# Performance work log

Measured on AMD Instinct MI355X. Metric: run time of the kernel, lower is better.

Reference implementation:

```python
import jax, jax.numpy as jnp
import numpy as np

# Dimensions inferred from the module (few-shot reweighted YOLOv2 region loss)
B, C, NA, NCPA = 64, 20, 5, 1          # batch, base classes, anchors, classes-per-anchor
H, W = 19, 19                           # feature map (608 input / stride 32)
T = 50                                  # cfg.max_boxes
THRESH = 0.6
COORD_SCALE = 1.0
CLASS_SCALE = 1.0
NB = B * C                              # per-class 'image' rows, as in the torch code
A4 = NA * H * W
EPS = 1e-12
BCE_EPS = 1e-7
ANCHORS = [[1.3221, 1.73145], [3.19275, 4.00944], [5.05587, 8.09892], [9.47112, 4.84053], [11.2364, 10.0071]]


def iou_xywh(x1, y1, w1, h1, x2, y2, w2, h2):
    # center-size IoU, matches darknet bbox_iou(x1y1x2y2=False)
    l = jnp.maximum(x1 - w1 * 0.5, x2 - w2 * 0.5)
    r = jnp.minimum(x1 + w1 * 0.5, x2 + w2 * 0.5)
    t = jnp.maximum(y1 - h1 * 0.5, y2 - h2 * 0.5)
    b = jnp.minimum(y1 + h1 * 0.5, y2 + h2 * 0.5)
    inter = jnp.clip(r - l, 0.0) * jnp.clip(b - t, 0.0)
    union = w1 * h1 + w2 * h2 - inter
    return inter / jnp.maximum(union, EPS)


def setup_inputs() -> dict:
    key = jax.random.key(0)
    k1, k2, k3, k4 = jax.random.split(key, 4)
    output = jax.random.normal(k1, (NB, NA * (5 + NCPA), H, W), jnp.float32) * 0.5
    # target rows: [cls, x, y, w, h] * T, coords in (0,1); x kept > 0 so all boxes are 'valid'
    cls_ids = jax.random.randint(k2, (B, C, T), 0, C).astype(jnp.float32)
    xy = jax.random.uniform(k3, (B, C, T, 2), minval=0.05, maxval=0.95)
    wh = jax.random.uniform(k4, (B, C, T, 2), minval=0.05, maxval=0.5)
    target = jnp.concatenate([cls_ids[..., None], xy, wh], axis=-1).reshape(B, C, T * 5)
    anchors = jnp.asarray(ANCHORS, jnp.float32)
    return {"output": output, "target": target, "anchors": anchors}


def _forward(output, target, anchors):
    target = jax.lax.stop_gradient(target)
    anchors = jax.lax.stop_gradient(anchors)
    out5 = output.reshape(NB, NA, 5 + NCPA, H, W)
    x = jax.nn.sigmoid(out5[:, :, 0])
    y = jax.nn.sigmoid(out5[:, :, 1])
    w = out5[:, :, 2]
    h = out5[:, :, 3]
    conf = jax.nn.sigmoid(out5[:, :, 4])
    # class logits regrouped to original batch: (B*NA*H*W, C)
    cls = out5[:, :, 5:5 + NCPA].reshape(NB, NA, H, W)
    cls_logits = cls.reshape(B, C, NA * H * W).transpose(0, 2, 1).reshape(-1, C)
    # decode pred boxes (detached, mirroring torch's use of .data)
    grid_x = jnp.arange(W, dtype=jnp.float32)[None, None, None, :]
    grid_y = jnp.arange(H, dtype=jnp.float32)[None, None, :, None]
    aw = anchors[:, 0][None, :, None, None]
    ah = anchors[:, 1][None, :, None, None]
    px = jax.lax.stop_gradient(x) + grid_x
    py = jax.lax.stop_gradient(y) + grid_y
    pw = jnp.exp(jax.lax.stop_gradient(w)) * aw
    ph = jnp.exp(jax.lax.stop_gradient(h)) * ah
    # ground-truth boxes per row
    tgt = target.reshape(NB, T, 5)
    cls_t = tgt[:, :, 0]
    gx = tgt[:, :, 1] * W
    gy = tgt[:, :, 2] * H
    gw = tgt[:, :, 3] * W
    gh = tgt[:, :, 4] * H
    # 'break on first zero x' semantics
    valid = jnp.cumprod((tgt[:, :, 1] != 0).astype(jnp.int32), axis=1) > 0
    # stage 1: zero conf_mask where any gt IoU > thresh (scan over T to avoid (NB,T,A4) blowup)
    pxf = px.reshape(NB, A4); pyf = py.reshape(NB, A4)
    pwf = pw.reshape(NB, A4); phf = ph.reshape(NB, A4)

    def iou_step(ci, xs):
        gxt, gyt, gwt, ght, vt = xs
        iou = iou_xywh(pxf, pyf, pwf, phf, gxt[:, None], gyt[:, None], gwt[:, None], ght[:, None])
        return jnp.maximum(ci, jnp.where(vt[:, None], iou, 0.0)), None

    cur_ious, _ = jax.lax.scan(iou_step, jnp.zeros((NB, A4), jnp.float32), (gx.T, gy.T, gw.T, gh.T, valid.T))
    conf_mask0 = jnp.where(cur_ious.reshape(NB, NA, H, W) > THRESH, 0.0, 1.0)
    # best anchor per gt by wh-only IoU
    inter = jnp.minimum(gw[..., None], anchors[:, 0]) * jnp.minimum(gh[..., None], anchors[:, 1])
    union = gw[..., None] * gh[..., None] + anchors[:, 0] * anchors[:, 1] - inter
    best_n = jnp.argmax(inter / jnp.maximum(union, EPS), axis=-1).astype(jnp.int32)  # (NB,T)
    gi = gx.astype(jnp.int32)
    gj = gy.astype(jnp.int32)
    # stage 2: ordered scatter of targets (later boxes overwrite earlier, as in the torch loops)
    binds = jnp.arange(NB)
    z = jnp.zeros((NB, NA, H, W), jnp.float32)
    # seen < 12800 branch: tx=ty=0.5, tw=th=0, coord_mask=1
    carry0 = (jnp.ones_like(z), z, conf_mask0, jnp.full_like(z, 0.5), jnp.full_like(z, 0.5), z, z, z, z)

    def tgt_step(carry, xs):
        cm, clm, cfm, tx, ty, tw, th, tconf, tcls = carry
        gxt, gyt, gwt, ght, bn, git, gjt, vt, ct = xs
        idx = (binds, bn, gjt, git)

        def upd(arr, val):
            return arr.at[idx].set(jnp.where(vt, val, arr[idx]))

        aw_b = anchors[bn, 0]
        ah_b = anchors[bn, 1]
        iou = iou_xywh(gxt, gyt, gwt, ght, px[idx], py[idx], pw[idx], ph[idx])
        cm = upd(cm, 1.0)
        clm = upd(clm, 1.0)
        cfm = upd(cfm, 1.0)
        tx = upd(tx, gxt - git.astype(jnp.float32))
        ty = upd(ty, gyt - gjt.astype(jnp.float32))
        tw = upd(tw, jnp.log(jnp.maximum(gwt, EPS) / aw_b))
        th = upd(th, jnp.log(jnp.maximum(ght, EPS) / ah_b))
        tconf = upd(tconf, iou)
        tcls = upd(tcls, ct)
        return (cm, clm, cfm, tx, ty, tw, th, tconf, tcls), None

    xs = (gx.T, gy.T, gw.T, gh.T, best_n.T, gi.T, gj.T, valid.T, cls_t.T)
    (coord_mask, cls_mask, conf_mask, tx, ty, tw, th, tconf, tcls), _ = jax.lax.scan(tgt_step, carry0, xs)
    # regroup per-class rows back to original batch (neg_ratio='full' -> counts[i] == C)
    cm_grp = cls_mask.reshape(B, C, NA, H, W).sum(axis=1)
    tcls_grp = tcls.reshape(B, C, NA, H, W).sum(axis=1)
    sel = (cm_grp == 1.0).reshape(-1)           # exclude colliding cells
    labels = tcls_grp.reshape(-1).astype(jnp.int32)

    def bce_mean(p, t):
        p = jnp.clip(p, BCE_EPS, 1.0 - BCE_EPS)
        return jnp.mean(-(t * jnp.log(p) + (1.0 - t) * jnp.log(1.0 - p)))

    loss_x = COORD_SCALE * bce_mean(x * coord_mask, tx * coord_mask)
    loss_y = COORD_SCALE * bce_mean(y * coord_mask, ty * coord_mask)
    loss_w = COORD_SCALE * 0.5 * jnp.mean((w * coord_mask - tw * coord_mask) ** 2)
    loss_h = COORD_SCALE * 0.5 * jnp.mean((h * coord_mask - th * coord_mask) ** 2)
    loss_conf = 0.5 * jnp.mean((conf * conf_mask - tconf * conf_mask) ** 2)
    logp = jax.nn.log_softmax(cls_logits, axis=-1)
    nll = -jnp.take_along_axis(logp, labels[:, None], axis=1)[:, 0]
    nsel = jnp.maximum(jnp.sum(sel.astype(jnp.float32)), 1.0)
    loss_cls = CLASS_SCALE * jnp.sum(jnp.where(sel, nll, 0.0)) / nsel
    return loss_x + loss_y + loss_w + loss_h + loss_conf + loss_cls


def reference(output, target, anchors):
    return _forward(output, target, anchors)
```

## Files before the change

kernel.cpp:

```cpp
#include <hip/hip_runtime.h>
#include <math.h>

constexpr int cB   = 64;
constexpr int cC   = 20;
constexpr int cNA  = 5;
constexpr int cH   = 19;
constexpr int cW   = 19;
constexpr int cT   = 50;
constexpr int cNB  = cB * cC;
constexpr int cHW  = cH * cW;
constexpr int cA4  = cNA * cHW;
constexpr int cCH  = cNA * 6;
constexpr long cNTOT = (long)cNB * cA4;
constexpr int cCLS_BLOCKS = cB * cNA;

__device__ __constant__ float cAW[cNA]   = {1.3221f, 3.19275f, 5.05587f, 9.47112f, 11.2364f};
__device__ __constant__ float cAH[cNA]   = {1.73145f, 4.00944f, 8.09892f, 4.84053f, 10.0071f};
__device__ __constant__ float cAREA[cNA] = {2.28930345f, 12.80114796f, 40.94706183f, 45.84455262f, 112.44377644f};
__device__ __constant__ float cLNAW[cNA] = {0.27920469f, 1.16088088f, 1.62060702f, 2.24822684f, 2.41915174f};
__device__ __constant__ float cLNAH[cNA] = {0.54896100f, 1.38865236f, 2.09173157f, 1.57701337f, 2.30329495f};

constexpr int ACC_BANKS = 64;
constexpr size_t OFF_CNT = 2560;
constexpr size_t OFF_ROW = 4096;
constexpr size_t ZERO_BYTES = OFF_ROW + (size_t)cB * cA4 * 4;

__device__ __forceinline__ float fexp(float x) {
    return __builtin_amdgcn_exp2f(x * 1.4426950408889634f);
}
__device__ __forceinline__ float flog(float x) {
    return __builtin_amdgcn_logf(x) * 0.6931471805599453f;
}
__device__ __forceinline__ float frcp(float x) { return __builtin_amdgcn_rcpf(x); }
__device__ __forceinline__ float fsigmoid(float x) { return frcp(1.0f + fexp(-x)); }

typedef _Float16 h2 __attribute__((ext_vector_type(2)));
union HU { unsigned u; h2 h; };
__device__ __forceinline__ unsigned splat2(float v) {
    HU x; _Float16 f = (_Float16)v; x.h[0] = f; x.h[1] = f; return x.u;
}
constexpr float cS = 1.2649110640673518f;

__launch_bounds__(256)
__global__ void k_main(const float* __restrict__ outp, const float* __restrict__ target,
                       int* __restrict__ rowenc, double* __restrict__ acc) {
    __shared__ int s_win[cA4];
    __shared__ int s_tc[cT];
    __shared__ __align__(16) unsigned s_box[cT][8];
    __shared__ __align__(16) float4 s_gt[cT];
    __shared__ double s_red[3][4];
    const int tid  = threadIdx.x;
    const int nb   = blockIdx.x >> 1;
    const int half = blockIdx.x & 1;
    const int base = (half << 10) + tid;
    const int b_   = nb / cC;
    const int c_   = nb - b_ * cC;
    const float* obase = outp + (size_t)nb * (cCH * cHW);

    for (int k = tid; k < cA4; k += 256) s_win[k] = -1;
    __syncthreads();

    if (tid < 64) {
        const int t = tid;
        float xr = 1.f, yr = 0.f, wr = 0.f, hr = 0.f;
        if (t < cT) {
            const float* tg = target + (size_t)nb * (cT * 5) + t * 5;
            xr = tg[1]; yr = tg[2]; wr = tg[3]; hr = tg[4];
        }
        unsigned long long nz = __ballot(xr != 0.0f);
        if (t < cT) {
            unsigned long long below = (2ull << t) - 1ull;
            bool valid = ((~nz) & below) == 0ull;
            float gx = xr * (float)cW, gy = yr * (float)cH;
            float gw = wr * (float)cW, gh = hr * (float)cH;
            s_gt[t] = make_float4(gx, gy, gw, gh);
            if (valid) {
                s_box[t][0] = splat2(cS * (gx - 0.5f * gw));
                s_box[t][1] = splat2(cS * (gx + 0.5f * gw));
                s_box[t][2] = splat2(cS * (gy - 0.5f * gh));
                s_box[t][3] = splat2(cS * (gy + 0.5f * gh));
                s_box[t][4] = splat2(-0.6f * (gw * gh));
                float garea = gw * gh;
                float best = -1.0f; int bn = 0;
                for (int n = 0; n < cNA; ++n) {
                    float inter = fminf(gw, cAW[n]) * fminf(gh, cAH[n]);
                    float uni   = garea + cAREA[n] - inter;
                    float r = inter / fmaxf(uni, 1e-12f);
                    if (r > best) { best = r; bn = n; }
                }
                int cell = bn * cHW + (int)gy * cW + (int)gx;
                s_tc[t] = cell;
                atomicMax(&s_win[cell], t);
            } else {
                s_box[t][0] = splat2(1e4f);  s_box[t][1] = splat2(-1e4f);
                s_box[t][2] = splat2(1e4f);  s_box[t][3] = splat2(-1e4f);
                s_box[t][4] = splat2(0.0f);
                s_tc[t] = -1;
            }
        }
    }
    __syncthreads();
    if (half == 0 && tid < cT) {
        int cell = s_tc[tid];
        if (cell >= 0 && s_win[cell] == tid)
            atomicAdd(&rowenc[b_ * cA4 + cell], (1 << 10) | (c_ * cT + tid));
    }

    h2 pl2[2], pr2[2], pt2[2], pb2[2], ov2[2], pa06h[2];
    float conf[4], tcf[4];
    unsigned wbits = 0;
    float bce = 0.0f, sq = 0.0f;
    const h2 z2 = { (_Float16)0.0f, (_Float16)0.0f };

    #pragma unroll
    for (int u = 0; u < 4; ++u) {
        int cell = base + (u << 8);
        bool a_  = cell < cA4;
        int cc   = a_ ? cell : (cA4 - 1);
        int na   = cc / cHW;
        int rem  = cc - na * cHW;
        int j    = rem / cW;
        int i    = rem - j * cW;
        const float* ob = obase + (size_t)(na * 6) * cHW + rem;
        float xl = ob[0], yl = ob[cHW], wl = ob[2*cHW], hl = ob[3*cHW], cl = ob[4*cHW];
        float aw = cAW[na], ah = cAH[na];
        float x  = fsigmoid(xl), y = fsigmoid(yl), cf = fsigmoid(cl);
        float px = x + (float)i, py = y + (float)j;
        float pw = fexp(wl) * aw, ph = fexp(hl) * ah;
        float l0 = px - 0.5f*pw, r0 = px + 0.5f*pw;
        float t0 = py - 0.5f*ph, b0 = py + 0.5f*ph;
        float pa = pw * ph;
        int p = u >> 1, s = u & 1;
        pl2[p][s] = (_Float16)(cS * l0);  pr2[p][s] = (_Float16)(cS * r0);
        pt2[p][s] = (_Float16)(cS * t0);  pb2[p][s] = (_Float16)(cS * b0);
        pa06h[p][s] = (_Float16)(0.6f * pa);
        ov2[p][s] = (_Float16)0.0f;
        conf[u] = cf; tcf[u] = 0.0f;

        float tx = 0.5f, ty = 0.5f, tw = 0.0f, th = 0.0f;
        int wt = s_win[cc];
        bool wfl = (wt >= 0) && a_;
        if (wfl) {
            wbits |= (1u << u);
            float4 g = s_gt[wt];
            float gx = g.x, gy = g.y, gw = g.z, gh = g.w;
            tx = gx - (float)i; ty = gy - (float)j;
            tw = flog(fmaxf(gw, 1e-12f)) - cLNAW[na];
            th = flog(fmaxf(gh, 1e-12f)) - cLNAH[na];
            float iw = fminf(r0, gx + 0.5f*gw) - fmaxf(l0, gx - 0.5f*gw);
            float ih = fminf(b0, gy + 0.5f*gh) - fmaxf(t0, gy - 0.5f*gh);
            iw = fmaxf(iw, 0.0f); ih = fmaxf(ih, 0.0f);
            float inter = iw * ih;
            float uni   = gw*gh + pa - inter;
            tcf[u] = inter * frcp(fmaxf(uni, 1e-12f));
        }
        if (a_) {
            float pc = fminf(fmaxf(x, 1e-7f), 1.0f - 1e-7f);
            bce += -(tx * flog(pc) + (1.0f - tx) * flog(1.0f - pc));
            pc = fminf(fmaxf(y, 1e-7f), 1.0f - 1e-7f);
            bce += -(ty * flog(pc) + (1.0f - ty) * flog(1.0f - pc));
            float dw = wl - tw, dh = hl - th;
            sq += dw*dw + dh*dh;
        }
    }

    #pragma unroll 10
    for (int t = 0; t < cT; ++t) {
        uint4 bx = *(const uint4*)&s_box[t][0];
        unsigned gv = s_box[t][4];
        HU a, b, c, d, e;
        a.u = bx.x; b.u = bx.y; c.u = bx.z; d.u = bx.w; e.u = gv;
        #pragma unroll
        for (int p = 0; p < 2; ++p) {
            h2 iw = __builtin_elementwise_min(pr2[p], b.h) - __builtin_elementwise_max(pl2[p], a.h);
            h2 ih = __builtin_elementwise_min(pb2[p], d.h) - __builtin_elementwise_max(pt2[p], c.h);
            iw = __builtin_elementwise_max(iw, z2);
            ih = __builtin_elementwise_max(ih, z2);
            ov2[p] = __builtin_elementwise_max(ov2[p], iw * ih + e.h);
        }
    }

    float sc = 0.0f;
    #pragma unroll
    for (int u = 0; u < 4; ++u) {
        int cell = base + (u << 8);
        if (cell >= cA4) continue;
        int p = u >> 1, s = u & 1;
        bool wfl  = (wbits >> u) & 1;
        bool over = ov2[p][s] > pa06h[p][s];
        float cm  = wfl ? 1.0f : (over ? 0.0f : 1.0f);
        float d   = (conf[u] - tcf[u]) * cm;
        sc += d * d;
    }

    double v0 = (double)bce, v1 = (double)sq, v2 = (double)sc;
    for (int off = 32; off > 0; off >>= 1) {
        v0 += __shfl_down(v0, off);
        v1 += __shfl_down(v1, off);
        v2 += __shfl_down(v2, off);
    }
    int lane = tid & 63, wid = tid >> 6;
    if (lane == 0) { s_red[0][wid] = v0; s_red[1][wid] = v1; s_red[2][wid] = v2; }
    __syncthreads();
    if (tid == 0) {
        double a0 = s_red[0][0] + s_red[0][1] + s_red[0][2] + s_red[0][3];
        double a1 = s_red[1][0] + s_red[1][1] + s_red[1][2] + s_red[1][3];
        double a2 = s_red[2][0] + s_red[2][1] + s_red[2][2] + s_red[2][3];
        int bank = blockIdx.x & (ACC_BANKS - 1);
        atomicAdd(&acc[0*ACC_BANKS + bank], a0);
        atomicAdd(&acc[1*ACC_BANKS + bank], a1);
        atomicAdd(&acc[2*ACC_BANKS + bank], a2);
    }
}

__launch_bounds__(384)
__global__ void k_cls(const float* __restrict__ outp, const float* __restrict__ target,
                      const int* __restrict__ rowenc, double* __restrict__ acc,
                      int* __restrict__ cnt, float* __restrict__ out) {
    __shared__ double s_red[2][6];
    __shared__ int s_last;
    const int tid = threadIdx.x;
    const int b   = blockIdx.x / cNA;
    const int na  = blockIdx.x - b * cNA;
    double nll = 0.0, ns = 0.0;
    if (tid < cHW) {
        const int rem = tid;
        const float* ob = outp + ((size_t)(b * cC) * cCH + na * 6 + 5) * cHW + rem;
        float l[cC]; float m = -1e30f;
        #pragma unroll
        for (int c = 0; c < cC; ++c) {
            l[c] = ob[(size_t)c * (cCH * cHW)];
            m = fmaxf(m, l[c]);
        }
        float s = 0.0f;
        #pragma unroll
        for (int c = 0; c < cC; ++c) s += fexp(l[c] - m);
        float lse = m + flog(s);
        int row = b * cA4 + na * cHW + rem;
        int v = rowenc[row];
        if ((v >> 10) == 1) {
            int payload = v & 1023;
            int selc = payload / cT;
            int selt = payload - selc * cT;
            int label = (int)target[((size_t)(b * cC + selc) * cT + selt) * 5];
            nll = (double)(lse - l[label]);
            ns  = 1.0;
        }
    }
    for (int off = 32; off > 0; off >>= 1) {
        nll += __shfl_down(nll, off);
        ns  += __shfl_down(ns, off);
    }
    int lane = tid & 63, wid = tid >> 6;
    if (lane == 0) { s_red[0][wid] = nll; s_red[1][wid] = ns; }
    __syncthreads();
    if (tid == 0) {
        double a0 = 0.0, a1 = 0.0;
        #pragma unroll
        for (int w = 0; w < 6; ++w) { a0 += s_red[0][w]; a1 += s_red[1][w]; }
        int bank = blockIdx.x & (ACC_BANKS - 1);
        atomicAdd(&acc[3*ACC_BANKS + bank], a0);
        atomicAdd(&acc[4*ACC_BANKS + bank], a1);
        __threadfence();
        s_last = (atomicAdd(cnt, 1) == cCLS_BLOCKS - 1);
    }
    __syncthreads();
    if (s_last && tid < 64) {
        __threadfence();
        double s[5];
        #pragma unroll
        for (int j = 0; j < 5; ++j) {
            double v = atomicAdd(&acc[j * ACC_BANKS + tid], 0.0);
            for (int off = 32; off > 0; off >>= 1) v += __shfl_down(v, off);
            s[j] = v;
        }
        if (tid == 0) {
            double Ninv = 1.0 / (double)cNTOT;
            double loss = s[0] * Ninv
                        + 0.5 * s[1] * Ninv
                        + 0.5 * s[2] * Ninv
                        + s[3] / fmax(s[4], 1.0);
            out[0] = (float)loss;
        }
    }
}

extern "C" void kernel_launch(void* const* d_in, const int* in_sizes, int n_in,
                              void* d_out, int out_size, void* d_ws, size_t ws_size,
                              hipStream_t stream) {
    const float* output = (const float*)d_in[0];
    const float* target = (const float*)d_in[1];
    char* ws = (char*)d_ws;
    double* acc    = (double*)ws;
    int*    cnt    = (int*)(ws + OFF_CNT);
    int*    rowenc = (int*)(ws + OFF_ROW);

    hipMemsetAsync(ws, 0, ZERO_BYTES, stream);

    k_main<<<cNB * 2, 256, 0, stream>>>(output, target, rowenc, acc);
    k_cls<<<cCLS_BLOCKS, 384, 0, stream>>>(output, target, rowenc, acc, cnt, (float*)d_out);
}
```

Before: 128.8 us.

## Rework main and class kernels: one block per row, precomputed targets, split softmax

Result: slower. 162.9 us (+26.4%).

```diff
diff --git a/kernel.cpp b/kernel.cpp
--- a/kernel.cpp
+++ b/kernel.cpp
@@ -12,7 +12,7 @@
 constexpr int cA4  = cNA * cHW;
 constexpr int cCH  = cNA * 6;
 constexpr long cNTOT = (long)cNB * cA4;
-constexpr int cCLS_BLOCKS = cB * cNA;
+constexpr int cCLS_BLOCKS = (cB * cA4 * 4) / 256;
 
 __device__ __constant__ float cAW[cNA]   = {1.3221f, 3.19275f, 5.05587f, 9.47112f, 11.2364f};
 __device__ __constant__ float cAH[cNA]   = {1.73145f, 4.00944f, 8.09892f, 4.84053f, 10.0071f};
@@ -41,18 +41,16 @@
 }
 constexpr float cS = 1.2649110640673518f;
 
-__launch_bounds__(256)
+__launch_bounds__(256, 5)
 __global__ void k_main(const float* __restrict__ outp, const float* __restrict__ target,
                        int* __restrict__ rowenc, double* __restrict__ acc) {
     __shared__ int s_win[cA4];
     __shared__ int s_tc[cT];
     __shared__ __align__(16) unsigned s_box[cT][8];
-    __shared__ __align__(16) float4 s_gt[cT];
+    __shared__ float s_tval[cT][6];
     __shared__ double s_red[3][4];
     const int tid  = threadIdx.x;
-    const int nb   = blockIdx.x >> 1;
-    const int half = blockIdx.x & 1;
-    const int base = (half << 10) + tid;
+    const int nb   = blockIdx.x;
     const int b_   = nb / cC;
     const int c_   = nb - b_ * cC;
     const float* obase = outp + (size_t)nb * (cCH * cHW);
@@ -73,7 +71,6 @@
             bool valid = ((~nz) & below) == 0ull;
             float gx = xr * (float)cW, gy = yr * (float)cH;
             float gw = wr * (float)cW, gh = hr * (float)cH;
-            s_gt[t] = make_float4(gx, gy, gw, gh);
             if (valid) {
                 s_box[t][0] = splat2(cS * (gx - 0.5f * gw));
                 s_box[t][1] = splat2(cS * (gx + 0.5f * gw));
@@ -88,9 +85,26 @@
                     float r = inter / fmaxf(uni, 1e-12f);
                     if (r > best) { best = r; bn = n; }
                 }
-                int cell = bn * cHW + (int)gy * cW + (int)gx;
+                int gi = (int)gx, gj = (int)gy;
+                int cell = bn * cHW + gj * cW + gi;
                 s_tc[t] = cell;
                 atomicMax(&s_win[cell], t);
+                const float* ob = obase + (size_t)(bn * 6) * cHW + gj * cW + gi;
+                float xl = ob[0], yl = ob[cHW], wl = ob[2*cHW], hl = ob[3*cHW];
+                float pxc = fsigmoid(xl) + (float)gi;
+                float pyc = fsigmoid(yl) + (float)gj;
+                float pw = fexp(wl) * cAW[bn], ph = fexp(hl) * cAH[bn];
+                float il = fmaxf(pxc - 0.5f*pw, gx - 0.5f*gw);
+                float ir = fminf(pxc + 0.5f*pw, gx + 0.5f*gw);
+                float it = fmaxf(pyc - 0.5f*ph, gy - 0.5f*gh);
+                float ib = fminf(pyc + 0.5f*ph, gy + 0.5f*gh);
+                float inter2 = fmaxf(ir - il, 0.0f) * fmaxf(ib - it, 0.0f);
+                float uni2   = pw * ph + gw * gh - inter2;
+                s_tval[t][0] = gx - (float)gi;
+                s_tval[t][1] = gy - (float)gj;
+                s_tval[t][2] = flog(fmaxf(gw, 1e-12f)) - cLNAW[bn];
+                s_tval[t][3] = flog(fmaxf(gh, 1e-12f)) - cLNAH[bn];
+                s_tval[t][4] = inter2 * frcp(fmaxf(uni2, 1e-12f));
             } else {
                 s_box[t][0] = splat2(1e4f);  s_box[t][1] = splat2(-1e4f);
                 s_box[t][2] = splat2(1e4f);  s_box[t][3] = splat2(-1e4f);
@@ -100,21 +114,22 @@
         }
     }
     __syncthreads();
-    if (half == 0 && tid < cT) {
+    if (tid < cT) {
         int cell = s_tc[tid];
         if (cell >= 0 && s_win[cell] == tid)
             atomicAdd(&rowenc[b_ * cA4 + cell], (1 << 10) | (c_ * cT + tid));
     }
 
-    h2 pl2[2], pr2[2], pt2[2], pb2[2], ov2[2], pa06h[2];
-    float conf[4], tcf[4];
+    h2 pl2[4], pr2[4], pt2[4], pb2[4], ov2[4], pa06h[4];
+    float conf[8], tcf[8];
     unsigned wbits = 0;
     float bce = 0.0f, sq = 0.0f;
     const h2 z2 = { (_Float16)0.0f, (_Float16)0.0f };
+    constexpr float cLN2 = 0.6931471805599453f;
 
     #pragma unroll
-    for (int u = 0; u < 4; ++u) {
-        int cell = base + (u << 8);
+    for (int u = 0; u < 8; ++u) {
+        int cell = tid + (u << 8);
         bool a_  = cell < cA4;
         int cc   = a_ ? cell : (cA4 - 1);
         int na   = cc / cHW;
@@ -123,8 +138,16 @@
         int i    = rem - j * cW;
         const float* ob = obase + (size_t)(na * 6) * cHW + rem;
         float xl = ob[0], yl = ob[cHW], wl = ob[2*cHW], hl = ob[3*cHW], cl = ob[4*cHW];
+        float Ex = __builtin_amdgcn_exp2f(-1.4426950408889634f * xl);
+        float Sx = 1.0f + Ex;
+        float x  = frcp(Sx);
+        float Lx = __builtin_amdgcn_logf(Sx);
+        float Ey = __builtin_amdgcn_exp2f(-1.4426950408889634f * yl);
+        float Sy = 1.0f + Ey;
+        float y  = frcp(Sy);
+        float Ly = __builtin_amdgcn_logf(Sy);
+        float cf = frcp(1.0f + fexp(-cl));
         float aw = cAW[na], ah = cAH[na];
-        float x  = fsigmoid(xl), y = fsigmoid(yl), cf = fsigmoid(cl);
         float px = x + (float)i, py = y + (float)j;
         float pw = fexp(wl) * aw, ph = fexp(hl) * ah;
         float l0 = px - 0.5f*pw, r0 = px + 0.5f*pw;
@@ -135,55 +158,45 @@
         pt2[p][s] = (_Float16)(cS * t0);  pb2[p][s] = (_Float16)(cS * b0);
         pa06h[p][s] = (_Float16)(0.6f * pa);
         ov2[p][s] = (_Float16)0.0f;
-        conf[u] = cf; tcf[u] = 0.0f;
-
-        float tx = 0.5f, ty = 0.5f, tw = 0.0f, th = 0.0f;
+        conf[u] = cf;
+
+        float tx = 0.5f, ty = 0.5f, tw = 0.0f, th = 0.0f, tc = 0.0f;
         int wt = s_win[cc];
         bool wfl = (wt >= 0) && a_;
         if (wfl) {
             wbits |= (1u << u);
-            float4 g = s_gt[wt];
-            float gx = g.x, gy = g.y, gw = g.z, gh = g.w;
-            tx = gx - (float)i; ty = gy - (float)j;
-            tw = flog(fmaxf(gw, 1e-12f)) - cLNAW[na];
-            th = flog(fmaxf(gh, 1e-12f)) - cLNAH[na];
-            float iw = fminf(r0, gx + 0.5f*gw) - fmaxf(l0, gx - 0.5f*gw);
-            float ih = fminf(b0, gy + 0.5f*gh) - fmaxf(t0, gy - 0.5f*gh);
-            iw = fmaxf(iw, 0.0f); ih = fmaxf(ih, 0.0f);
-            float inter = iw * ih;
-            float uni   = gw*gh + pa - inter;
-            tcf[u] = inter * frcp(fmaxf(uni, 1e-12f));
-        }
+            tx = s_tval[wt][0]; ty = s_tval[wt][1];
+            tw = s_tval[wt][2]; th = s_tval[wt][3];
+            tc = s_tval[wt][4];
+        }
+        tcf[u] = tc;
         if (a_) {
-            float pc = fminf(fmaxf(x, 1e-7f), 1.0f - 1e-7f);
-            bce += -(tx * flog(pc) + (1.0f - tx) * flog(1.0f - pc));
-            pc = fminf(fmaxf(y, 1e-7f), 1.0f - 1e-7f);
-            bce += -(ty * flog(pc) + (1.0f - ty) * flog(1.0f - pc));
+            bce += (1.0f - tx) * xl + cLN2 * Lx;
+            bce += (1.0f - ty) * yl + cLN2 * Ly;
             float dw = wl - tw, dh = hl - th;
             sq += dw*dw + dh*dh;
         }
     }
 
-    #pragma unroll 10
+    #pragma unroll 2
     for (int t = 0; t < cT; ++t) {
         uint4 bx = *(const uint4*)&s_box[t][0];
         unsigned gv = s_box[t][4];
         HU a, b, c, d, e;
         a.u = bx.x; b.u = bx.y; c.u = bx.z; d.u = bx.w; e.u = gv;
         #pragma unroll
-        for (int p = 0; p < 2; ++p) {
+        for (int p = 0; p < 4; ++p) {
             h2 iw = __builtin_elementwise_min(pr2[p], b.h) - __builtin_elementwise_max(pl2[p], a.h);
             h2 ih = __builtin_elementwise_min(pb2[p], d.h) - __builtin_elementwise_max(pt2[p], c.h);
             iw = __builtin_elementwise_max(iw, z2);
-            ih = __builtin_elementwise_max(ih, z2);
             ov2[p] = __builtin_elementwise_max(ov2[p], iw * ih + e.h);
         }
     }
 
     float sc = 0.0f;
     #pragma unroll
-    for (int u = 0; u < 4; ++u) {
-        int cell = base + (u << 8);
+    for (int u = 0; u < 8; ++u) {
+        int cell = tid + (u << 8);
         if (cell >= cA4) continue;
         int p = u >> 1, s = u & 1;
         bool wfl  = (wbits >> u) & 1;
@@ -213,40 +226,51 @@
     }
 }
 
-__launch_bounds__(384)
+__launch_bounds__(256)
 __global__ void k_cls(const float* __restrict__ outp, const float* __restrict__ target,
                       const int* __restrict__ rowenc, double* __restrict__ acc,
                       int* __restrict__ cnt, float* __restrict__ out) {
-    __shared__ double s_red[2][6];
+    __shared__ double s_red[2][4];
+    __shared__ double s_fin[5];
     __shared__ int s_last;
-    const int tid = threadIdx.x;
-    const int b   = blockIdx.x / cNA;
-    const int na  = blockIdx.x - b * cNA;
+    const int tid  = threadIdx.x;
+    const int gid  = blockIdx.x * 256 + tid;
+    const int cellId = gid >> 2;
+    const int q    = gid & 3;
+    const int b    = cellId / cA4;
+    const int idx  = cellId - b * cA4;
+    const int na   = idx / cHW;
+    const int rem  = idx - na * cHW;
+    const size_t cstep = (size_t)cCH * cHW;
+    const float* pb = outp + ((size_t)b * cC * cCH + na * 6 + 5) * cHW + rem;
+
+    float l[5];
+    #pragma unroll
+    for (int k = 0; k < 5; ++k) l[k] = pb[(size_t)(5*q + k) * cstep];
+    float m = fmaxf(fmaxf(fmaxf(l[0], l[1]), fmaxf(l[2], l[3])), l[4]);
+    m = fmaxf(m, __shfl_xor(m, 1));
+    m = fmaxf(m, __shfl_xor(m, 2));
+    float s = 0.0f;
+    #pragma unroll
+    for (int k = 0; k < 5; ++k) s += fexp(l[k] - m);
+    s += __shfl_xor(s, 1);
+    s += __shfl_xor(s, 2);
+    float lse = m + flog(s);
+
     double nll = 0.0, ns = 0.0;
-    if (tid < cHW) {
-        const int rem = tid;
-        const float* ob = outp + ((size_t)(b * cC) * cCH + na * 6 + 5) * cHW + rem;
-        float l[cC]; float m = -1e30f;
-        #pragma unroll
-        for (int c = 0; c < cC; ++c) {
-            l[c] = ob[(size_t)c * (cCH * cHW)];
-            m = fmaxf(m, l[c]);
-        }
-        float s = 0.0f;
-        #pragma unroll
-        for (int c = 0; c < cC; ++c) s += fexp(l[c] - m);
-        float lse = m + flog(s);
-        int row = b * cA4 + na * cHW + rem;
-        int v = rowenc[row];
-        if ((v >> 10) == 1) {
-            int payload = v & 1023;
-            int selc = payload / cT;
-            int selt = payload - selc * cT;
-            int label = (int)target[((size_t)(b * cC + selc) * cT + selt) * 5];
-            nll = (double)(lse - l[label]);
+    int v = rowenc[cellId];
+    if ((v >> 10) == 1) {
+        int payload = v & 1023;
+        int selc = payload / cT;
+        int selt = payload - selc * cT;
+        int label = (int)target[((size_t)(b * cC + selc) * cT + selt) * 5];
+        int lo = label - 5 * q;
+        if (lo >= 0 && lo < 5) {
+            nll = (double)(lse - l[lo]);
             ns  = 1.0;
         }
     }
+
     for (int off = 32; off > 0; off >>= 1) {
         nll += __shfl_down(nll, off);
         ns  += __shfl_down(ns, off);
@@ -255,9 +279,8 @@
     if (lane == 0) { s_red[0][wid] = nll; s_red[1][wid] = ns; }
     __syncthreads();
     if (tid == 0) {
-        double a0 = 0.0, a1 = 0.0;
-        #pragma unroll
-        for (int w = 0; w < 6; ++w) { a0 += s_red[0][w]; a1 += s_red[1][w]; }
+        double a0 = s_red[0][0] + s_red[0][1] + s_red[0][2] + s_red[0][3];
+        double a1 = s_red[1][0] + s_red[1][1] + s_red[1][2] + s_red[1][3];
         int bank = blockIdx.x & (ACC_BANKS - 1);
         atomicAdd(&acc[3*ACC_BANKS + bank], a0);
         atomicAdd(&acc[4*ACC_BANKS + bank], a1);
@@ -265,21 +288,22 @@
         s_last = (atomicAdd(cnt, 1) == cCLS_BLOCKS - 1);
     }
     __syncthreads();
-    if (s_last && tid < 64) {
+    if (s_last) {
         __threadfence();
-        double s[5];
-        #pragma unroll
-        for (int j = 0; j < 5; ++j) {
-            double v = atomicAdd(&acc[j * ACC_BANKS + tid], 0.0);
-            for (int off = 32; off > 0; off >>= 1) v += __shfl_down(v, off);
-            s[j] = v;
-        }
+        double va = atomicAdd(&acc[tid], 0.0);
+        double vb = (tid < 64) ? atomicAdd(&acc[256 + tid], 0.0) : 0.0;
+        for (int off = 32; off > 0; off >>= 1) {
+            va += __shfl_down(va, off);
+            vb += __shfl_down(vb, off);
+        }
+        if (lane == 0) { s_fin[wid] = va; if (wid == 0) s_fin[4] = vb; }
+        __syncthreads();
         if (tid == 0) {
             double Ninv = 1.0 / (double)cNTOT;
-            double loss = s[0] * Ninv
-                        + 0.5 * s[1] * Ninv
-                        + 0.5 * s[2] * Ninv
-                        + s[3] / fmax(s[4], 1.0);
+            double loss = s_fin[0] * Ninv
+                        + 0.5 * s_fin[1] * Ninv
+                        + 0.5 * s_fin[2] * Ninv
+                        + s_fin[3] / fmax(s_fin[4], 1.0);
             out[0] = (float)loss;
         }
     }
@@ -297,6 +321,6 @@
 
     hipMemsetAsync(ws, 0, ZERO_BYTES, stream);
 
-    k_main<<<cNB * 2, 256, 0, stream>>>(output, target, rowenc, acc);
-    k_cls<<<cCLS_BLOCKS, 384, 0, stream>>>(output, target, rowenc, acc, cnt, (float*)d_out);
-}
+    k_main<<<cNB, 256, 0, stream>>>(output, target, rowenc, acc);
+    k_cls<<<cCLS_BLOCKS, 256, 0, stream>>>(output, target, rowenc, acc, cnt, (float*)d_out);
+}
```
